# Optimization experiments

Hardware: AMD Instinct MI355X
Metric: run time of the kernel (lower is better)

## Reference

```python
import jax, jax.numpy as jnp
import numpy as np
from jax import lax

D_MODEL = 2048
D_SSM = 4096          # expand * d_model
D_STATE = 128
NHEADS = 64
HEADDIM = 64          # D_SSM // NHEADS
NGROUPS = 1
D_CONV = 4
CHUNK = 64
D_IN_PROJ = 2 * D_SSM + 2 * NGROUPS * D_STATE + NHEADS   # 8512
CONV_DIM = D_SSM + 2 * NGROUPS * D_STATE                 # 4352
EPS = 1e-5


def setup_inputs() -> dict:
    key = jax.random.key(0)
    ks = jax.random.split(key, 10)
    B, L = 2, 4096
    u = jax.random.normal(ks[0], (B, L, D_MODEL), dtype=jnp.float32)
    W_in = jax.random.normal(ks[1], (D_IN_PROJ, D_MODEL), dtype=jnp.float32) * 0.02
    conv_w = jax.random.normal(ks[2], (CONV_DIM, D_CONV), dtype=jnp.float32) * 0.2
    conv_b = jax.random.normal(ks[3], (CONV_DIM,), dtype=jnp.float32) * 0.02
    # dt_bias ~ inverse-softplus of dt in [1e-3, 0.1]
    dt = jnp.exp(jax.random.uniform(ks[4], (NHEADS,), minval=np.log(1e-3), maxval=np.log(0.1)))
    dt_bias = dt + jnp.log(-jnp.expm1(-dt))
    # A ~ U(1, 16) -> A_log
    A_log = jnp.log(jax.random.uniform(ks[5], (NHEADS,), minval=1.0, maxval=16.0))
    D = jnp.ones((NHEADS,), dtype=jnp.float32)
    norm_weight = jnp.ones((D_SSM,), dtype=jnp.float32)
    W_out = jax.random.normal(ks[6], (D_MODEL, D_SSM), dtype=jnp.float32) * 0.02
    return {"u": u, "W_in": W_in, "conv_w": conv_w, "conv_b": conv_b,
            "dt_bias": dt_bias, "A_log": A_log, "D": D,
            "norm_weight": norm_weight, "W_out": W_out}


def _segsum(x):
    """x: [..., l] -> [..., l, l] with out[i,j] = sum_{k=j+1..i} x[k], -inf above diag."""
    l = x.shape[-1]
    cs = jnp.cumsum(x, axis=-1)
    seg = cs[..., :, None] - cs[..., None, :]
    mask = jnp.tril(jnp.ones((l, l), dtype=bool))
    return jnp.where(mask, seg, -jnp.inf)


def reference(u, W_in, conv_w, conv_b, dt_bias, A_log, D, norm_weight, W_out):
    b, L, _ = u.shape
    zxbcdt = jnp.einsum('bld,ed->ble', u, W_in)          # [b, L, 8512]
    z = zxbcdt[..., :D_SSM]                              # gate
    xBC = zxbcdt[..., D_SSM:D_SSM + CONV_DIM]
    dt = zxbcdt[..., -NHEADS:]                           # [b, L, h]

    # depthwise causal conv1d (kernel D_CONV) + SiLU
    xp = jnp.pad(xBC, ((0, 0), (D_CONV - 1, 0), (0, 0)))
    conv = conv_b
    for k in range(D_CONV):
        conv = conv + xp[:, k:k + L, :] * conv_w[:, k]
    xBC = jax.nn.silu(conv)

    x = xBC[..., :D_SSM].reshape(b, L, NHEADS, HEADDIM)
    Bm = xBC[..., D_SSM:D_SSM + D_STATE]                 # ngroups=1: [b, L, n]
    Cm = xBC[..., D_SSM + D_STATE:]

    dt = jax.nn.softplus(dt + dt_bias)                   # [b, L, h]
    A = -jnp.exp(A_log)                                  # [h]

    c = L // CHUNK
    xc = x.reshape(b, c, CHUNK, NHEADS, HEADDIM)
    dtc = dt.reshape(b, c, CHUNK, NHEADS)
    Bc = Bm.reshape(b, c, CHUNK, D_STATE)
    Cc = Cm.reshape(b, c, CHUNK, D_STATE)

    dA = dtc * A                                         # [b, c, l, h]
    A_cum = jnp.cumsum(dA, axis=2)

    # intra-chunk (diagonal) blocks
    Lmat = jnp.exp(_segsum(dA.transpose(0, 1, 3, 2)))    # [b, c, h, l, s]
    CB = jnp.einsum('bcln,bcsn->bcls', Cc, Bc)           # [b, c, l, s]
    Y_diag = jnp.einsum('bcls,bchls,bcsh,bcshp->bclhp', CB, Lmat, dtc, xc)

    # per-chunk final states
    decay_states = jnp.exp(A_cum[:, :, -1:, :] - A_cum)  # [b, c, l, h]
    states = jnp.einsum('bcln,bclh,bclhp->bchpn', Bc, decay_states * dtc, xc)

    # inter-chunk recurrence over chunks
    chunk_decay = jnp.exp(A_cum[:, :, -1, :])            # [b, c, h]

    def step(carry, inp):
        s, cd = inp                                      # s: [b,h,p,n], cd: [b,h]
        new = carry * cd[:, :, None, None] + s
        return new, carry                                # emit state BEFORE this chunk

    init = jnp.zeros((b, NHEADS, HEADDIM, D_STATE), dtype=u.dtype)
    _, prev = lax.scan(step, init, (states.transpose(1, 0, 2, 3, 4),
                                    chunk_decay.transpose(1, 0, 2)))
    prev = prev.transpose(1, 0, 2, 3, 4)                 # [b, c, h, p, n]

    Y_off = jnp.einsum('bcln,bchpn,bclh->bclhp', Cc, prev, jnp.exp(A_cum))

    y = (Y_diag + Y_off + xc * D[None, None, None, :, None]).reshape(b, L, D_SSM)

    # gated RMSNorm (norm_before_gate=False): rmsnorm(y * silu(z)) * weight
    yg = y * jax.nn.silu(z)
    var = jnp.mean(yg * yg, axis=-1, keepdims=True)
    y = yg * lax.rsqrt(var + EPS) * norm_weight

    return jnp.einsum('bld,ed->ble', y, W_out)
```

## Files before the change

kernel.cpp:

```cpp
#include <hip/hip_runtime.h>

typedef unsigned short u16;
typedef __attribute__((ext_vector_type(4))) float f4;
typedef __attribute__((ext_vector_type(8))) __bf16 bf16x8;
typedef __attribute__((ext_vector_type(4))) float f32x4;

#define D_MODEL 2048
#define D_SSM 4096
#define D_STATE 128
#define NHEADS 64
#define HEADDIM 64
#define CHUNK 64
#define LTOT 4096
#define NB 2
#define CONV_DIM 4352
#define XBC_LD 4480
#define LOG2E 1.4426950408889634f

__device__ inline float bf2f(unsigned v) { return __uint_as_float(v << 16); }
__device__ inline u16 f2bf(float f) {
    unsigned u = __float_as_uint(f);
    unsigned r = (u + 0x7fffu + ((u >> 16) & 1u)) >> 16;
    return (u16)r;
}
__device__ inline unsigned pack2(float a, float b) {
    return (unsigned)f2bf(a) | ((unsigned)f2bf(b) << 16);
}
__device__ inline float fexp2(float x) {
    float r;
    asm("v_exp_f32 %0, %1" : "=v"(r) : "v"(x));
    return r;
}
__device__ inline unsigned cvtpk(float lo, float hi) {
    unsigned r;
    asm("v_cvt_pk_bf16_f32 %0, %1, %2" : "=v"(r) : "v"(lo), "v"(hi));
    return r;
}
__device__ inline void gload_lds16(const void* g, void* l) {
    __builtin_amdgcn_global_load_lds((const __attribute__((address_space(1))) void*)g,
                                     (__attribute__((address_space(3))) void*)l, 16, 0, 0);
}
__device__ inline f32x4 mfma16(bf16x8 a, bf16x8 b, f32x4 c) {
    return __builtin_amdgcn_mfma_f32_16x16x32_bf16(a, b, c, 0, 0, 0);
}

__global__ __launch_bounds__(256) void tobf16_kernel(const float* __restrict__ src,
                                                     u16* __restrict__ dst, int n4) {
    int i = blockIdx.x * 256 + threadIdx.x;
    if (i < n4) {
        f4 v = ((const f4*)src)[i];
        uint2 pk;
        pk.x = pack2(v[0], v[1]);
        pk.y = pack2(v[2], v[3]);
        ((uint2*)dst)[i] = pk;
    }
}

__global__ __launch_bounds__(256) void winpad_kernel(const float* __restrict__ src,
                                                     u16* __restrict__ dst) {
    int i = blockIdx.x * 256 + threadIdx.x;
    if (i >= (8704 * 2048 / 4)) return;
    int col4 = i & 511;
    int row = i >> 9;
    f4 v = {0.f, 0.f, 0.f, 0.f};
    if (row < 8512) v = ((const f4*)src)[row * 512 + col4];
    uint2 pk;
    pk.x = pack2(v[0], v[1]);
    pk.y = pack2(v[2], v[3]);
    ((uint2*)dst)[i] = pk;
}

template <int OUT_BF16>
__global__ __launch_bounds__(512, 1) void gemm256(const u16* __restrict__ A,
                                                  const u16* __restrict__ Bm,
                                                  void* __restrict__ Cp,
                                                  int K, int ldC, int Nreal) {
    __shared__ __align__(16) u16 lds[2][32768];

    int t = threadIdx.x;
    int w = t >> 6, lane = t & 63;
    int fm = lane & 15, fq = lane >> 4;
    int wm = w >> 2, wn = w & 3;

    int gx = gridDim.x;
    int nwg = gx * gridDim.y;
    int orig = blockIdx.y * gx + blockIdx.x;
    int wg = (orig & 7) * (nwg >> 3) + (orig >> 3);
    int blockN = (wg % gx) * 256;
    int blockM = (wg / gx) * 256;

    int srow = t >> 3;
    int scol = (((t & 7) ^ (srow & 7)) << 3);
    const u16* Asrc = A + (size_t)(blockM + srow) * K + scol;
    const u16* Bsrc = Bm + (size_t)(blockN + srow) * K + scol;

#define STAGE(buf, isB, half, tile)                                              \
    do {                                                                         \
        const u16* _s = ((isB) ? Bsrc : Asrc) + (size_t)(tile) * 64 +            \
                        (size_t)((half) * 128) * K;                              \
        u16* _d = &lds[buf][(isB) * 16384 + (half) * 8192 + t * 8];              \
        gload_lds16(_s, _d);                                                     \
        gload_lds16(_s + (size_t)64 * K, _d + 4096);                             \
    } while (0)

    int nt = K >> 6;
    STAGE(0, 0, 0, 0); STAGE(0, 1, 0, 0);
    STAGE(0, 0, 1, 0); STAGE(0, 1, 1, 0);
    STAGE(1, 0, 0, 1); STAGE(1, 1, 0, 1);

    f32x4 acc[8][4] = {};
    int lro = fm * 64;
    int ko0 = ((fq ^ (fm & 7)) << 3);
    int ko1 = (((4 + fq) ^ (fm & 7)) << 3);

    asm volatile("s_waitcnt vmcnt(8)" ::: "memory");
    __builtin_amdgcn_s_barrier();

    for (int kt = 0; kt < nt; ++kt) {
        int d = kt & 1, e = d ^ 1;
        const u16* aH0 = &lds[d][wm * 4096 + lro];
        const u16* aH1 = aH0 + 8192;
        const u16* bH0 = &lds[d][16384 + wn * 2048 + lro];
        const u16* bH1 = bH0 + 8192;
        bf16x8 af[4][2], bfr[2][2];

#pragma unroll
        for (int i = 0; i < 4; ++i) {
            af[i][0] = *(const bf16x8*)(aH0 + i * 1024 + ko0);
            af[i][1] = *(const bf16x8*)(aH0 + i * 1024 + ko1);
        }
#pragma unroll
        for (int j = 0; j < 2; ++j) {
            bfr[j][0] = *(const bf16x8*)(bH0 + j * 1024 + ko0);
            bfr[j][1] = *(const bf16x8*)(bH0 + j * 1024 + ko1);
        }
        if (kt + 1 < nt) STAGE(e, 0, 1, kt + 1);
        __builtin_amdgcn_s_barrier();
        __builtin_amdgcn_s_setprio(1);
#pragma unroll
        for (int i = 0; i < 4; ++i)
#pragma unroll
            for (int j = 0; j < 2; ++j) {
                acc[i][j] = mfma16(af[i][0], bfr[j][0], acc[i][j]);
                acc[i][j] = mfma16(af[i][1], bfr[j][1], acc[i][j]);
            }
        __builtin_amdgcn_s_setprio(0);
        if (kt == nt - 1) asm volatile("s_waitcnt vmcnt(0)" ::: "memory");
        else              asm volatile("s_waitcnt vmcnt(6)" ::: "memory");
        __builtin_amdgcn_s_barrier();

#pragma unroll
        for (int j = 0; j < 2; ++j) {
            bfr[j][0] = *(const bf16x8*)(bH1 + j * 1024 + ko0);
            bfr[j][1] = *(const bf16x8*)(bH1 + j * 1024 + ko1);
        }
        if (kt + 1 < nt) STAGE(e, 1, 1, kt + 1);
        __builtin_amdgcn_s_barrier();
        __builtin_amdgcn_s_setprio(1);
#pragma unroll
        for (int i = 0; i < 4; ++i)
#pragma unroll
            for (int j = 0; j < 2; ++j) {
                acc[i][2 + j] = mfma16(af[i][0], bfr[j][0], acc[i][2 + j]);
                acc[i][2 + j] = mfma16(af[i][1], bfr[j][1], acc[i][2 + j]);
            }
        __builtin_amdgcn_s_setprio(0);
        __builtin_amdgcn_s_barrier();

#pragma unroll
        for (int i = 0; i < 4; ++i) {
            af[i][0] = *(const bf16x8*)(aH1 + i * 1024 + ko0);
            af[i][1] = *(const bf16x8*)(aH1 + i * 1024 + ko1);
        }
#pragma unroll
        for (int j = 0; j < 2; ++j) {
            bfr[j][0] = *(const bf16x8*)(bH0 + j * 1024 + ko0);
            bfr[j][1] = *(const bf16x8*)(bH0 + j * 1024 + ko1);
        }
        if (kt + 2 < nt) STAGE(d, 0, 0, kt + 2);
        __builtin_amdgcn_s_barrier();
        __builtin_amdgcn_s_setprio(1);
#pragma unroll
        for (int i = 0; i < 4; ++i)
#pragma unroll
            for (int j = 0; j < 2; ++j) {
                acc[4 + i][j] = mfma16(af[i][0], bfr[j][0], acc[4 + i][j]);
                acc[4 + i][j] = mfma16(af[i][1], bfr[j][1], acc[4 + i][j]);
            }
        __builtin_amdgcn_s_setprio(0);
        __builtin_amdgcn_s_barrier();

#pragma unroll
        for (int j = 0; j < 2; ++j) {
            bfr[j][0] = *(const bf16x8*)(bH1 + j * 1024 + ko0);
            bfr[j][1] = *(const bf16x8*)(bH1 + j * 1024 + ko1);
        }
        if (kt + 2 < nt) STAGE(d, 1, 0, kt + 2);
        __builtin_amdgcn_s_barrier();
        __builtin_amdgcn_s_setprio(1);
#pragma unroll
        for (int i = 0; i < 4; ++i)
#pragma unroll
            for (int j = 0; j < 2; ++j) {
                acc[4 + i][2 + j] = mfma16(af[i][0], bfr[j][0], acc[4 + i][2 + j]);
                acc[4 + i][2 + j] = mfma16(af[i][1], bfr[j][1], acc[4 + i][2 + j]);
            }
        __builtin_amdgcn_s_setprio(0);
        if (kt == nt - 2)      asm volatile("s_waitcnt vmcnt(4)" ::: "memory");
        else if (kt < nt - 2)  asm volatile("s_waitcnt vmcnt(8)" ::: "memory");
        __builtin_amdgcn_s_barrier();
    }
#undef STAGE

#pragma unroll
    for (int i = 0; i < 8; ++i) {
        int rbase = (i < 4) ? (wm * 64 + i * 16) : (128 + wm * 64 + (i - 4) * 16);
        int row = blockM + rbase + fq * 4;
#pragma unroll
        for (int j = 0; j < 4; ++j) {
            int cbase = (j < 2) ? (wn * 32 + j * 16) : (128 + wn * 32 + (j - 2) * 16);
            int col = blockN + cbase + fm;
            if (col < Nreal) {
                if (OUT_BF16) {
                    u16* C = (u16*)Cp;
#pragma unroll
                    for (int r = 0; r < 4; ++r)
                        C[(size_t)(row + r) * ldC + col] = f2bf(acc[i][j][r]);
                } else {
                    float* C = (float*)Cp;
#pragma unroll
                    for (int r = 0; r < 4; ++r)
                        C[(size_t)(row + r) * ldC + col] = acc[i][j][r];
                }
            }
        }
    }
}

__global__ __launch_bounds__(256) void conv_kernel(const u16* __restrict__ xbcdt,
                                                   const float* __restrict__ conv_w,
                                                   const float* __restrict__ conv_b,
                                                   u16* __restrict__ convO) {
    int ch = blockIdx.x * 256 + threadIdx.x;
    int row = blockIdx.y;
    int l = row & (LTOT - 1);
    f4 w = *(const f4*)&conv_w[ch * 4];
    float acc = conv_b[ch];
#pragma unroll
    for (int k = 0; k < 4; ++k) {
        int ls = l - 3 + k;
        if (ls >= 0) acc += bf2f(xbcdt[(size_t)(row - 3 + k) * XBC_LD + ch]) * w[k];
    }
    convO[(size_t)row * CONV_DIM + ch] = f2bf(acc / (1.f + __expf(-acc)));
}

__global__ __launch_bounds__(256) void dt_kernel(const u16* __restrict__ xbcdt,
                                                 const float* __restrict__ dt_bias,
                                                 float* __restrict__ dtp) {
    int idx = blockIdx.x * 256 + threadIdx.x;
    if (idx >= NB * LTOT * NHEADS) return;
    int row = idx >> 6, h = idx & 63;
    float x = bf2f(xbcdt[(size_t)row * XBC_LD + CONV_DIM + h]) + dt_bias[h];
    dtp[idx] = (x > 15.f) ? x : log1pf(__expf(x));
}

__global__ __launch_bounds__(256) void cb_kernel(const u16* __restrict__ convO,
                                                 float* __restrict__ CBb) {
    __shared__ u16 Bt[128 * 68];
    __shared__ u16 Ct[128 * 68];
    int bc = blockIdx.x;
    int c = bc & 63, b = bc >> 6;
    int rowbase = b * LTOT + c * CHUNK;
    int t = threadIdx.x;
#pragma unroll
    for (int i = 0; i < 32; i++) {
        int idx = i * 256 + t;
        int s = idx >> 7, n = idx & 127;
        Bt[n * 68 + s] = convO[(size_t)(rowbase + s) * CONV_DIM + D_SSM + n];
        Ct[n * 68 + s] = convO[(size_t)(rowbase + s) * CONV_DIM + D_SSM + D_STATE + n];
    }
    __syncthreads();
    int sq = t & 15, lq = t >> 4;
    f4 acc[4] = {};
#pragma unroll 4
    for (int n = 0; n < 128; n++) {
        ushort4 bv = *(const ushort4*)&Bt[n * 68 + sq * 4];
        ushort4 cv = *(const ushort4*)&Ct[n * 68 + lq * 4];
        f4 bf;
        bf[0] = bf2f(bv.x); bf[1] = bf2f(bv.y); bf[2] = bf2f(bv.z); bf[3] = bf2f(bv.w);
        float c0 = bf2f(cv.x), c1 = bf2f(cv.y), c2 = bf2f(cv.z), c3 = bf2f(cv.w);
        acc[0] += c0 * bf; acc[1] += c1 * bf; acc[2] += c2 * bf; acc[3] += c3 * bf;
    }
    float* outb = CBb + (size_t)bc * 4096;
#pragma unroll
    for (int j = 0; j < 4; j++) *(f4*)&outb[(lq * 4 + j) * 64 + sq * 4] = acc[j];
}

__global__ __launch_bounds__(256, 2) void ssm_mfma(const u16* __restrict__ convO,
                                                   const float* __restrict__ dtp,
                                                   const float* __restrict__ CBb,
                                                   const float* __restrict__ A_log,
                                                   const float* __restrict__ Dvec,
                                                   u16* __restrict__ ybf) {
    __shared__ __align__(16) u16 xT[2][16 * 72];
    __shared__ __align__(16) u16 BT[2][128 * 64];
    __shared__ __align__(16) u16 Sd[2][16 * 136];
    __shared__ __align__(16) float scal[2][256];

    int t = threadIdx.x;
    int w = t >> 6, lane = t & 63;
    int z = blockIdx.x;
    int pg = z & 3, h = (z >> 2) & 63, b = z >> 8;
    int pbase = h * 64 + pg * 16;
    float Ah2 = -__expf(A_log[h]) * LOG2E;
    float Dh = Dvec[h];

    int fm = lane & 15;
    int fq = lane >> 4;
    int fk = fq * 8;
    int sl = t & 63;
    int sq = t >> 6;
    int lq = t & 15;
    int no = t >> 4;

    f32x4 sacc[2] = {};

    const float* CBbase = CBb + (size_t)(b * 64) * 4096;
    int yl = 16 * w + fm;
    int btc0 = (32 * w + fm) * 64;
    int fm7 = fm & 7;

    bf16x8 afr[4];
    f4 cbr[2][2];
    {
        int rowbase = b * LTOT;
        const u16* rowp = convO + (size_t)rowbase * CONV_DIM;
        const u16* Cg = rowp + (size_t)yl * CONV_DIM + D_SSM + D_STATE;
#pragma unroll
        for (int kk = 0; kk < 4; ++kk) afr[kk] = *(const bf16x8*)(Cg + kk * 32 + fk);
        const float* CBrow = CBbase + yl * 64;
#pragma unroll
        for (int kk = 0; kk < 2; ++kk) {
            cbr[kk][0] = *(const f4*)&CBrow[kk * 32 + fk];
            cbr[kk][1] = *(const f4*)&CBrow[kk * 32 + fk + 4];
        }
        if (t < 64) {
            float dtv = dtp[(size_t)(rowbase + t) * 64 + h];
            float v = dtv * Ah2;
#pragma unroll
            for (int off = 1; off < 64; off <<= 1) {
                float pv = __shfl_up(v, off, 64);
                if (t >= off) v += pv;
            }
            float alast = __shfl(v, 63, 64);
            scal[0][t] = dtv;
            scal[0][64 + t] = v;
            scal[0][128 + t] = dtv * fexp2(alast - v);
            scal[0][192 + t] = fexp2(v);
        }
        ushort4 xv = *(const ushort4*)(rowp + (size_t)sl * CONV_DIM + pbase + sq * 4);
        xT[0][(sq * 4 + 0) * 72 + sl] = xv.x;
        xT[0][(sq * 4 + 1) * 72 + sl] = xv.y;
        xT[0][(sq * 4 + 2) * 72 + sl] = xv.z;
        xT[0][(sq * 4 + 3) * 72 + sl] = xv.w;
        {
            const u16* bp = rowp + D_SSM + no * 8;
            union { uint4 v; unsigned ww[4]; } q[4];
#pragma unroll
            for (int r = 0; r < 4; ++r) q[r].v = *(const uint4*)(bp + (size_t)(4 * lq + r) * CONV_DIM);
            int base = no * 512 + (lq & 1) * 4;
            int lqh = lq >> 1;
#pragma unroll
            for (int j = 0; j < 8; ++j) {
                unsigned sel = (j & 1) ? 0x07060302u : 0x05040100u;
                uint2 pk;
                pk.x = __builtin_amdgcn_perm(q[1].ww[j >> 1], q[0].ww[j >> 1], sel);
                pk.y = __builtin_amdgcn_perm(q[3].ww[j >> 1], q[2].ww[j >> 1], sel);
                *(uint2*)&BT[0][base + j * 64 + ((lqh ^ j) << 3)] = pk;
            }
        }
#pragma unroll
        for (int nt = 0; nt < 2; ++nt)
#pragma unroll
            for (int r = 0; r < 4; ++r)
                Sd[0][(fq * 4 + r) * 136 + 32 * w + 16 * nt + fm] = 0;
        __syncthreads();
    }

    f4 ydef = {0.f, 0.f, 0.f, 0.f};
    int cur = 0;
    for (int c = 0; c < 64; ++c, cur ^= 1) {
        int rowbase = b * LTOT + c * CHUNK;
        const u16* rowp = convO + (size_t)rowbase * CONV_DIM;

        if (c > 0) {
            unsigned y01 = cvtpk(ydef[0], ydef[1]);
            unsigned y23 = cvtpk(ydef[2], ydef[3]);
            u16* yp = ybf + (size_t)(rowbase - CHUNK + 16 * w + fq * 4) * D_SSM + pbase + fm;
            yp[0] = (u16)y01;
            yp[D_SSM] = (u16)(y01 >> 16);
            yp[2 * D_SSM] = (u16)y23;
            yp[3 * D_SSM] = (u16)(y23 >> 16);
        }

        bf16x8 afr_n[4] = {};
        f4 cbr_n[2][2] = {};
        uint4 bv0 = {}, bv1 = {}, bv2 = {}, bv3 = {};
        ushort4 xv = {0, 0, 0, 0};
        float dtv = 0.f;
        if (c < 63) {
            const u16* rowp1 = rowp + (size_t)CHUNK * CONV_DIM;
            const u16* Cg = rowp1 + (size_t)yl * CONV_DIM + D_SSM + D_STATE;
#pragma unroll
            for (int kk = 0; kk < 4; ++kk) afr_n[kk] = *(const bf16x8*)(Cg + kk * 32 + fk);
            const float* CBrow = CBbase + (size_t)(c + 1) * 4096 + yl * 64;
#pragma unroll
            for (int kk = 0; kk < 2; ++kk) {
                cbr_n[kk][0] = *(const f4*)&CBrow[kk * 32 + fk];
                cbr_n[kk][1] = *(const f4*)&CBrow[kk * 32 + fk + 4];
            }
            const u16* bp = rowp1 + D_SSM + no * 8;
            bv0 = *(const uint4*)(bp + (size_t)(4 * lq + 0) * CONV_DIM);
            bv1 = *(const uint4*)(bp + (size_t)(4 * lq + 1) * CONV_DIM);
            bv2 = *(const uint4*)(bp + (size_t)(4 * lq + 2) * CONV_DIM);
            bv3 = *(const uint4*)(bp + (size_t)(4 * lq + 3) * CONV_DIM);
            xv = *(const ushort4*)(rowp1 + (size_t)sl * CONV_DIM + pbase + sq * 4);
            if (t < 64) dtv = dtp[(size_t)(rowbase + CHUNK + t) * 64 + h];
        }

        const float* sc = scal[cur];
        const u16* xTc = xT[cur];
        const u16* BTc = BT[cur];
        const u16* Sdc = Sd[cur];

        union { uint4 v; u16 us[8]; bf16x8 bv; } xx0, xx1;
        xx0.v = *(const uint4*)&xTc[fm * 72 + fk];
        xx1.v = *(const uint4*)&xTc[fm * 72 + 32 + fk];
        ushort4 xe = *(const ushort4*)&xTc[fm * 72 + 16 * w + fq * 4];
        f4 els4 = *(const f4*)&sc[192 + 16 * w + fq * 4];
        float acl = sc[64 + yl];
        float cd = sc[192 + 63];
        f4 ac00 = *(const f4*)&sc[64 + fk], ac01 = *(const f4*)&sc[64 + fk + 4];
        f4 ac10 = *(const f4*)&sc[96 + fk], ac11 = *(const f4*)&sc[96 + fk + 4];
        f4 dt00 = *(const f4*)&sc[fk], dt01 = *(const f4*)&sc[fk + 4];
        f4 dt10 = *(const f4*)&sc[32 + fk], dt11 = *(const f4*)&sc[32 + fk + 4];
        f4 w00 = *(const f4*)&sc[128 + fk], w01 = *(const f4*)&sc[128 + fk + 4];
        f4 w10 = *(const f4*)&sc[160 + fk], w11 = *(const f4*)&sc[160 + fk + 4];
        bf16x8 sdf0 = *(const bf16x8*)&Sdc[fm * 136 + fk];
        bf16x8 sdf1 = *(const bf16x8*)&Sdc[fm * 136 + 32 + fk];
        bf16x8 sdf2 = *(const bf16x8*)&Sdc[fm * 136 + 64 + fk];
        bf16x8 sdf3 = *(const bf16x8*)&Sdc[fm * 136 + 96 + fk];
        int pb0 = (fq ^ fm7) << 3;
        int pb1 = ((4 + fq) ^ fm7) << 3;
        bf16x8 btf00 = *(const bf16x8*)&BTc[btc0 + pb0];
        bf16x8 btf01 = *(const bf16x8*)&BTc[btc0 + 1024 + pb0];
        bf16x8 btf10 = *(const bf16x8*)&BTc[btc0 + pb1];
        bf16x8 btf11 = *(const bf16x8*)&BTc[btc0 + 1024 + pb1];

        f32x4 ydia = {0.f, 0.f, 0.f, 0.f};
        {
            union { unsigned u[4]; bf16x8 v; } gu;
            float g[8];
#pragma unroll
            for (int j = 0; j < 4; ++j) {
                int s = fk + j;
                g[j] = (s <= yl) ? cbr[0][0][j] * fexp2(acl - ac00[j]) * dt00[j] : 0.f;
            }
#pragma unroll
            for (int j = 0; j < 4; ++j) {
                int s = fk + 4 + j;
                g[4 + j] = (s <= yl) ? cbr[0][1][j] * fexp2(acl - ac01[j]) * dt01[j] : 0.f;
            }
            gu.u[0] = cvtpk(g[0], g[1]);
            gu.u[1] = cvtpk(g[2], g[3]);
            gu.u[2] = cvtpk(g[4], g[5]);
            gu.u[3] = cvtpk(g[6], g[7]);
            ydia = __builtin_amdgcn_mfma_f32_16x16x32_bf16(gu.v, xx0.bv, ydia, 0, 0, 0);
#pragma unroll
            for (int j = 0; j < 4; ++j) {
                int s = 32 + fk + j;
                g[j] = (s <= yl) ? cbr[1][0][j] * fexp2(acl - ac10[j]) * dt10[j] : 0.f;
            }
#pragma unroll
            for (int j = 0; j < 4; ++j) {
                int s = 32 + fk + 4 + j;
                g[4 + j] = (s <= yl) ? cbr[1][1][j] * fexp2(acl - ac11[j]) * dt11[j] : 0.f;
            }
            gu.u[0] = cvtpk(g[0], g[1]);
            gu.u[1] = cvtpk(g[2], g[3]);
            gu.u[2] = cvtpk(g[4], g[5]);
            gu.u[3] = cvtpk(g[6], g[7]);
            ydia = __builtin_amdgcn_mfma_f32_16x16x32_bf16(gu.v, xx1.bv, ydia, 0, 0, 0);
        }

        sacc[0] *= cd;
        sacc[1] *= cd;
        {
            union { unsigned u[4]; bf16x8 v; } au;
            float xf[8];
#pragma unroll
            for (int j = 0; j < 8; ++j) xf[j] = bf2f(xx0.us[j]);
            au.u[0] = cvtpk(xf[0] * w00[0], xf[1] * w00[1]);
            au.u[1] = cvtpk(xf[2] * w00[2], xf[3] * w00[3]);
            au.u[2] = cvtpk(xf[4] * w01[0], xf[5] * w01[1]);
            au.u[3] = cvtpk(xf[6] * w01[2], xf[7] * w01[3]);
            sacc[0] = __builtin_amdgcn_mfma_f32_16x16x32_bf16(au.v, btf00, sacc[0], 0, 0, 0);
            sacc[1] = __builtin_amdgcn_mfma_f32_16x16x32_bf16(au.v, btf01, sacc[1], 0, 0, 0);
#pragma unroll
            for (int j = 0; j < 8; ++j) xf[j] = bf2f(xx1.us[j]);
            au.u[0] = cvtpk(xf[0] * w10[0], xf[1] * w10[1]);
            au.u[1] = cvtpk(xf[2] * w10[2], xf[3] * w10[3]);
            au.u[2] = cvtpk(xf[4] * w11[0], xf[5] * w11[1]);
            au.u[3] = cvtpk(xf[6] * w11[2], xf[7] * w11[3]);
            sacc[0] = __builtin_amdgcn_mfma_f32_16x16x32_bf16(au.v, btf10, sacc[0], 0, 0, 0);
            sacc[1] = __builtin_amdgcn_mfma_f32_16x16x32_bf16(au.v, btf11, sacc[1], 0, 0, 0);
        }

        f32x4 yoff = {0.f, 0.f, 0.f, 0.f};
        yoff = __builtin_amdgcn_mfma_f32_16x16x32_bf16(afr[0], sdf0, yoff, 0, 0, 0);
        yoff = __builtin_amdgcn_mfma_f32_16x16x32_bf16(afr[1], sdf1, yoff, 0, 0, 0);
        yoff = __builtin_amdgcn_mfma_f32_16x16x32_bf16(afr[2], sdf2, yoff, 0, 0, 0);
        yoff = __builtin_amdgcn_mfma_f32_16x16x32_bf16(afr[3], sdf3, yoff, 0, 0, 0);

        {
            float xf0 = bf2f(xe.x), xf1 = bf2f(xe.y), xf2 = bf2f(xe.z), xf3 = bf2f(xe.w);
            ydef[0] = yoff[0] * els4[0] + ydia[0] + Dh * xf0;
            ydef[1] = yoff[1] * els4[1] + ydia[1] + Dh * xf1;
            ydef[2] = yoff[2] * els4[2] + ydia[2] + Dh * xf2;
            ydef[3] = yoff[3] * els4[3] + ydia[3] + Dh * xf3;
        }

        if (c < 63) {
            int nxt = cur ^ 1;
            if (t < 64) {
                float v = dtv * Ah2;
#pragma unroll
                for (int off = 1; off < 64; off <<= 1) {
                    float pv = __shfl_up(v, off, 64);
                    if (t >= off) v += pv;
                }
                float alast = __shfl(v, 63, 64);
                scal[nxt][t] = dtv;
                scal[nxt][64 + t] = v;
                scal[nxt][128 + t] = dtv * fexp2(alast - v);
                scal[nxt][192 + t] = fexp2(v);
            }
            xT[nxt][(sq * 4 + 0) * 72 + sl] = xv.x;
            xT[nxt][(sq * 4 + 1) * 72 + sl] = xv.y;
            xT[nxt][(sq * 4 + 2) * 72 + sl] = xv.z;
            xT[nxt][(sq * 4 + 3) * 72 + sl] = xv.w;
            {
                union { uint4 v; unsigned ww[4]; } q0, q1, q2, q3;
                q0.v = bv0; q1.v = bv1; q2.v = bv2; q3.v = bv3;
                int base = no * 512 + (lq & 1) * 4;
                int lqh = lq >> 1;
#pragma unroll
                for (int j = 0; j < 8; ++j) {
                    unsigned sel = (j & 1) ? 0x07060302u : 0x05040100u;
                    uint2 pk;
                    pk.x = __builtin_amdgcn_perm(q1.ww[j >> 1], q0.ww[j >> 1], sel);
                    pk.y = __builtin_amdgcn_perm(q3.ww[j >> 1], q2.ww[j >> 1], sel);
                    *(uint2*)&BT[nxt][base + j * 64 + ((lqh ^ j) << 3)] = pk;
                }
            }
#pragma unroll
            for (int nt = 0; nt < 2; ++nt) {
                unsigned p01 = cvtpk(sacc[nt][0], sacc[nt][1]);
                unsigned p23 = cvtpk(sacc[nt][2], sacc[nt][3]);
                int colb = 32 * w + 16 * nt + fm;
                Sd[nxt][(fq * 4 + 0) * 136 + colb] = (u16)p01;
                Sd[nxt][(fq * 4 + 1) * 136 + colb] = (u16)(p01 >> 16);
                Sd[nxt][(fq * 4 + 2) * 136 + colb] = (u16)p23;
                Sd[nxt][(fq * 4 + 3) * 136 + colb] = (u16)(p23 >> 16);
            }
        }
        __syncthreads();

#pragma unroll
        for (int kk = 0; kk < 4; ++kk) afr[kk] = afr_n[kk];
#pragma unroll
        for (int kk = 0; kk < 2; ++kk) {
            cbr[kk][0] = cbr_n[kk][0];
            cbr[kk][1] = cbr_n[kk][1];
        }
    }

    {
        unsigned y01 = cvtpk(ydef[0], ydef[1]);
        unsigned y23 = cvtpk(ydef[2], ydef[3]);
        u16* yp = ybf + (size_t)(b * LTOT + 63 * CHUNK + 16 * w + fq * 4) * D_SSM + pbase + fm;
        yp[0] = (u16)y01;
        yp[D_SSM] = (u16)(y01 >> 16);
        yp[2 * D_SSM] = (u16)y23;
        yp[3 * D_SSM] = (u16)(y23 >> 16);
    }
}

__global__ __launch_bounds__(256) void gate_norm(const u16* __restrict__ zbf,
                                                 const float* __restrict__ normw,
                                                 u16* __restrict__ ybf) {
    int row = blockIdx.x, t = threadIdx.x;
    const uint2* y2 = (const uint2*)(ybf + (size_t)row * D_SSM);
    const uint2* z2 = (const uint2*)(zbf + (size_t)row * D_SSM);
    f4 yg[4];
    float ss = 0.f;
#pragma unroll
    for (int i = 0; i < 4; ++i) {
        int idx = i * 256 + t;
        uint2 yv = y2[idx], zv = z2[idx];
        float ya[4] = {bf2f(yv.x & 0xffffu), bf2f(yv.x >> 16), bf2f(yv.y & 0xffffu), bf2f(yv.y >> 16)};
        float za[4] = {bf2f(zv.x & 0xffffu), bf2f(zv.x >> 16), bf2f(zv.y & 0xffffu), bf2f(zv.y >> 16)};
        f4 g;
#pragma unroll
        for (int k = 0; k < 4; ++k) {
            float sz = za[k] / (1.f + __expf(-za[k]));
            g[k] = ya[k] * sz;
            ss += g[k] * g[k];
        }
        yg[i] = g;
    }
#pragma unroll
    for (int off = 32; off; off >>= 1) ss += __shfl_down(ss, off, 64);
    __shared__ float red[4];
    if ((t & 63) == 0) red[t >> 6] = ss;
    __syncthreads();
    float tot = red[0] + red[1] + red[2] + red[3];
    float scale = rsqrtf(tot / (float)D_SSM + 1e-5f);
    const f4* nw4 = (const f4*)normw;
    uint2* out = (uint2*)(ybf + (size_t)row * D_SSM);
#pragma unroll
    for (int i = 0; i < 4; ++i) {
        int idx = i * 256 + t;
        f4 v = yg[i] * scale * nw4[idx];
        uint2 pk;
        pk.x = pack2(v[0], v[1]);
        pk.y = pack2(v[2], v[3]);
        out[idx] = pk;
    }
}

extern "C" void kernel_launch(void* const* d_in, const int* in_sizes, int n_in,
                              void* d_out, int out_size, void* d_ws, size_t ws_size,
                              hipStream_t stream) {
    const float* u = (const float*)d_in[0];
    const float* W_in = (const float*)d_in[1];
    const float* conv_w = (const float*)d_in[2];
    const float* conv_b = (const float*)d_in[3];
    const float* dt_bias = (const float*)d_in[4];
    const float* A_log = (const float*)d_in[5];
    const float* Dv = (const float*)d_in[6];
    const float* normw = (const float*)d_in[7];
    const float* W_out = (const float*)d_in[8];
    float* out = (float*)d_out;
    char* ws = (char*)d_ws;

    u16* z_bf = (u16*)(ws + 0ULL);
    u16* xbcdt = (u16*)(ws + 67108864ULL);
    u16* y_bf = xbcdt;
    u16* convO = (u16*)(ws + 140509184ULL);
    u16* u_bf = convO;
    u16* win_bf = (u16*)(ws + 174063616ULL);
    u16* wout_bf = convO;
    float* dtp = (float*)(ws + 211812352ULL);
    float* CBb = (float*)(ws + 213909504ULL);

    tobf16_kernel<<<16384, 256, 0, stream>>>(u, u_bf, 4194304);
    winpad_kernel<<<17408, 256, 0, stream>>>(W_in, win_bf);
    gemm256<1><<<dim3(16, 32), 512, 0, stream>>>(u_bf, win_bf, z_bf, 2048, 4096, 4096);
    gemm256<1><<<dim3(18, 32), 512, 0, stream>>>(u_bf, win_bf + (size_t)4096 * 2048, xbcdt, 2048, XBC_LD, 4480);
    conv_kernel<<<dim3(17, 8192), 256, 0, stream>>>(xbcdt, conv_w, conv_b, convO);
    dt_kernel<<<2048, 256, 0, stream>>>(xbcdt, dt_bias, dtp);
    cb_kernel<<<128, 256, 0, stream>>>(convO, CBb);
    ssm_mfma<<<512, 256, 0, stream>>>(convO, dtp, CBb, A_log, Dv, y_bf);
    tobf16_kernel<<<8192, 256, 0, stream>>>(W_out, wout_bf, 2097152);
    gate_norm<<<8192, 256, 0, stream>>>(z_bf, normw, y_bf);
    gemm256<0><<<dim3(8, 32), 512, 0, stream>>>(y_bf, wout_bf, out, 4096, 2048, 2048);
}
```

Measured before the change: 972.6 us.

## Merge in-projection GEMMs, reuse B fragments, remap XCD swizzle, batch conv rows

The z and xBC/dt projection GEMMs become one launch whose epilogue routes each column tile to the right output buffer. This removes one launch and the tail imbalance of two separate grids. The block-to-XCD mapping now gives each XCD contiguous M tiles so it can share A in L2. B fragments are held in separate registers and reused for both A halves, which cuts LDS reads at the cost of more VGPRs. The conv kernel computes 8 consecutive rows per thread and reuses the overlapping inputs.

```diff
diff --git a/kernel.cpp b/kernel.cpp
--- a/kernel.cpp
+++ b/kernel.cpp
@@ -70,10 +70,11 @@
     ((uint2*)dst)[i] = pk;
 }
 
-template <int OUT_BF16>
+template <int MODE>
 __global__ __launch_bounds__(512, 1) void gemm256(const u16* __restrict__ A,
                                                   const u16* __restrict__ Bm,
                                                   void* __restrict__ Cp,
+                                                  void* __restrict__ Cp2,
                                                   int K, int ldC, int Nreal) {
     __shared__ __align__(16) u16 lds[2][32768];
 
@@ -82,12 +83,10 @@
     int fm = lane & 15, fq = lane >> 4;
     int wm = w >> 2, wn = w & 3;
 
-    int gx = gridDim.x;
-    int nwg = gx * gridDim.y;
-    int orig = blockIdx.y * gx + blockIdx.x;
-    int wg = (orig & 7) * (nwg >> 3) + (orig >> 3);
-    int blockN = (wg % gx) * 256;
-    int blockM = (wg / gx) * 256;
+    int orig = blockIdx.y * gridDim.x + blockIdx.x;
+    int xcd = orig & 7, s = orig >> 3;
+    int blockM = (xcd * 4 + (s & 3)) * 256;
+    int blockN = (s >> 2) * 256;
 
     int srow = t >> 3;
     int scol = (((t & 7) ^ (srow & 7)) << 3);
@@ -122,7 +121,7 @@
         const u16* aH1 = aH0 + 8192;
         const u16* bH0 = &lds[d][16384 + wn * 2048 + lro];
         const u16* bH1 = bH0 + 8192;
-        bf16x8 af[4][2], bfr[2][2];
+        bf16x8 af[4][2], b0[2][2], b1[2][2];
 
 #pragma unroll
         for (int i = 0; i < 4; ++i) {
@@ -131,8 +130,8 @@
         }
 #pragma unroll
         for (int j = 0; j < 2; ++j) {
-            bfr[j][0] = *(const bf16x8*)(bH0 + j * 1024 + ko0);
-            bfr[j][1] = *(const bf16x8*)(bH0 + j * 1024 + ko1);
+            b0[j][0] = *(const bf16x8*)(bH0 + j * 1024 + ko0);
+            b0[j][1] = *(const bf16x8*)(bH0 + j * 1024 + ko1);
         }
         if (kt + 1 < nt) STAGE(e, 0, 1, kt + 1);
         __builtin_amdgcn_s_barrier();
@@ -141,8 +140,8 @@
         for (int i = 0; i < 4; ++i)
 #pragma unroll
             for (int j = 0; j < 2; ++j) {
-                acc[i][j] = mfma16(af[i][0], bfr[j][0], acc[i][j]);
-                acc[i][j] = mfma16(af[i][1], bfr[j][1], acc[i][j]);
+                acc[i][j] = mfma16(af[i][0], b0[j][0], acc[i][j]);
+                acc[i][j] = mfma16(af[i][1], b0[j][1], acc[i][j]);
             }
         __builtin_amdgcn_s_setprio(0);
         if (kt == nt - 1) asm volatile("s_waitcnt vmcnt(0)" ::: "memory");
@@ -151,8 +150,8 @@
 
 #pragma unroll
         for (int j = 0; j < 2; ++j) {
-            bfr[j][0] = *(const bf16x8*)(bH1 + j * 1024 + ko0);
-            bfr[j][1] = *(const bf16x8*)(bH1 + j * 1024 + ko1);
+            b1[j][0] = *(const bf16x8*)(bH1 + j * 1024 + ko0);
+            b1[j][1] = *(const bf16x8*)(bH1 + j * 1024 + ko1);
         }
         if (kt + 1 < nt) STAGE(e, 1, 1, kt + 1);
         __builtin_amdgcn_s_barrier();
@@ -161,8 +160,8 @@
         for (int i = 0; i < 4; ++i)
 #pragma unroll
             for (int j = 0; j < 2; ++j) {
-                acc[i][2 + j] = mfma16(af[i][0], bfr[j][0], acc[i][2 + j]);
-                acc[i][2 + j] = mfma16(af[i][1], bfr[j][1], acc[i][2 + j]);
+                acc[i][2 + j] = mfma16(af[i][0], b1[j][0], acc[i][2 + j]);
+                acc[i][2 + j] = mfma16(af[i][1], b1[j][1], acc[i][2 + j]);
             }
         __builtin_amdgcn_s_setprio(0);
         __builtin_amdgcn_s_barrier();
@@ -172,11 +171,6 @@
             af[i][0] = *(const bf16x8*)(aH1 + i * 1024 + ko0);
             af[i][1] = *(const bf16x8*)(aH1 + i * 1024 + ko1);
         }
-#pragma unroll
-        for (int j = 0; j < 2; ++j) {
-            bfr[j][0] = *(const bf16x8*)(bH0 + j * 1024 + ko0);
-            bfr[j][1] = *(const bf16x8*)(bH0 + j * 1024 + ko1);
-        }
         if (kt + 2 < nt) STAGE(d, 0, 0, kt + 2);
         __builtin_amdgcn_s_barrier();
         __builtin_amdgcn_s_setprio(1);
@@ -184,17 +178,12 @@
         for (int i = 0; i < 4; ++i)
 #pragma unroll
             for (int j = 0; j < 2; ++j) {
-                acc[4 + i][j] = mfma16(af[i][0], bfr[j][0], acc[4 + i][j]);
-                acc[4 + i][j] = mfma16(af[i][1], bfr[j][1], acc[4 + i][j]);
+                acc[4 + i][j] = mfma16(af[i][0], b0[j][0], acc[4 + i][j]);
+                acc[4 + i][j] = mfma16(af[i][1], b0[j][1], acc[4 + i][j]);
             }
         __builtin_amdgcn_s_setprio(0);
         __builtin_amdgcn_s_barrier();
 
-#pragma unroll
-        for (int j = 0; j < 2; ++j) {
-            bfr[j][0] = *(const bf16x8*)(bH1 + j * 1024 + ko0);
-            bfr[j][1] = *(const bf16x8*)(bH1 + j * 1024 + ko1);
-        }
         if (kt + 2 < nt) STAGE(d, 1, 0, kt + 2);
         __builtin_amdgcn_s_barrier();
         __builtin_amdgcn_s_setprio(1);
@@ -202,8 +191,8 @@
         for (int i = 0; i < 4; ++i)
 #pragma unroll
             for (int j = 0; j < 2; ++j) {
-                acc[4 + i][2 + j] = mfma16(af[i][0], bfr[j][0], acc[4 + i][2 + j]);
-                acc[4 + i][2 + j] = mfma16(af[i][1], bfr[j][1], acc[4 + i][2 + j]);
+                acc[4 + i][2 + j] = mfma16(af[i][0], b1[j][0], acc[4 + i][2 + j]);
+                acc[4 + i][2 + j] = mfma16(af[i][1], b1[j][1], acc[4 + i][2 + j]);
             }
         __builtin_amdgcn_s_setprio(0);
         if (kt == nt - 2)      asm volatile("s_waitcnt vmcnt(4)" ::: "memory");
@@ -212,6 +201,12 @@
     }
 #undef STAGE
 
+    u16* Cb16 = 0;
+    int ldb = 0, coff = 0;
+    if (MODE == 2) {
+        if (blockN < 4096) { Cb16 = (u16*)Cp;  ldb = 4096; coff = blockN; }
+        else               { Cb16 = (u16*)Cp2; ldb = 4480; coff = blockN - 4096; }
+    }
 #pragma unroll
     for (int i = 0; i < 8; ++i) {
         int rbase = (i < 4) ? (wm * 64 + i * 16) : (128 + wm * 64 + (i - 4) * 16);
@@ -219,14 +214,16 @@
 #pragma unroll
         for (int j = 0; j < 4; ++j) {
             int cbase = (j < 2) ? (wn * 32 + j * 16) : (128 + wn * 32 + (j - 2) * 16);
-            int col = blockN + cbase + fm;
-            if (col < Nreal) {
-                if (OUT_BF16) {
-                    u16* C = (u16*)Cp;
+            if (MODE == 2) {
+                int col = coff + cbase + fm;
+                if (col < ldb) {
 #pragma unroll
                     for (int r = 0; r < 4; ++r)
-                        C[(size_t)(row + r) * ldC + col] = f2bf(acc[i][j][r]);
-                } else {
+                        Cb16[(size_t)(row + r) * ldb + col] = f2bf(acc[i][j][r]);
+                }
+            } else {
+                int col = blockN + cbase + fm;
+                if (col < Nreal) {
                     float* C = (float*)Cp;
 #pragma unroll
                     for (int r = 0; r < 4; ++r)
@@ -242,16 +239,21 @@
                                                    const float* __restrict__ conv_b,
                                                    u16* __restrict__ convO) {
     int ch = blockIdx.x * 256 + threadIdx.x;
-    int row = blockIdx.y;
-    int l = row & (LTOT - 1);
-    f4 w = *(const f4*)&conv_w[ch * 4];
-    float acc = conv_b[ch];
-#pragma unroll
-    for (int k = 0; k < 4; ++k) {
-        int ls = l - 3 + k;
-        if (ls >= 0) acc += bf2f(xbcdt[(size_t)(row - 3 + k) * XBC_LD + ch]) * w[k];
-    }
-    convO[(size_t)row * CONV_DIM + ch] = f2bf(acc / (1.f + __expf(-acc)));
+    int r0 = blockIdx.y * 8;
+    int l0 = r0 & (LTOT - 1);
+    f4 wv = *(const f4*)&conv_w[ch * 4];
+    float bias = conv_b[ch];
+    float xv[11];
+#pragma unroll
+    for (int j = 0; j < 11; ++j) {
+        int dj = j - 3;
+        xv[j] = (l0 + dj >= 0) ? bf2f(xbcdt[(size_t)(r0 + dj) * XBC_LD + ch]) : 0.f;
+    }
+#pragma unroll
+    for (int i = 0; i < 8; ++i) {
+        float acc = bias + xv[i] * wv[0] + xv[i + 1] * wv[1] + xv[i + 2] * wv[2] + xv[i + 3] * wv[3];
+        convO[(size_t)(r0 + i) * CONV_DIM + ch] = f2bf(acc / (1.f + __expf(-acc)));
+    }
 }
 
 __global__ __launch_bounds__(256) void dt_kernel(const u16* __restrict__ xbcdt,
@@ -666,13 +668,12 @@
 
     tobf16_kernel<<<16384, 256, 0, stream>>>(u, u_bf, 4194304);
     winpad_kernel<<<17408, 256, 0, stream>>>(W_in, win_bf);
-    gemm256<1><<<dim3(16, 32), 512, 0, stream>>>(u_bf, win_bf, z_bf, 2048, 4096, 4096);
-    gemm256<1><<<dim3(18, 32), 512, 0, stream>>>(u_bf, win_bf + (size_t)4096 * 2048, xbcdt, 2048, XBC_LD, 4480);
-    conv_kernel<<<dim3(17, 8192), 256, 0, stream>>>(xbcdt, conv_w, conv_b, convO);
+    gemm256<2><<<dim3(34, 32), 512, 0, stream>>>(u_bf, win_bf, z_bf, xbcdt, 2048, 0, 8576);
+    conv_kernel<<<dim3(17, 1024), 256, 0, stream>>>(xbcdt, conv_w, conv_b, convO);
     dt_kernel<<<2048, 256, 0, stream>>>(xbcdt, dt_bias, dtp);
     cb_kernel<<<128, 256, 0, stream>>>(convO, CBb);
     ssm_mfma<<<512, 256, 0, stream>>>(convO, dtp, CBb, A_log, Dv, y_bf);
     tobf16_kernel<<<8192, 256, 0, stream>>>(W_out, wout_bf, 2097152);
     gate_norm<<<8192, 256, 0, stream>>>(z_bf, normw, y_bf);
-    gemm256<0><<<dim3(8, 32), 512, 0, stream>>>(y_bf, wout_bf, out, 4096, 2048, 2048);
-}
+    gemm256<0><<<dim3(8, 32), 512, 0, stream>>>(y_bf, wout_bf, out, nullptr, 4096, 2048, 2048);
+}
```

After: 855.1 us. 12.1% less time.
